# Performance work log

Measured on AMD Instinct MI355X. Metric: run time of the kernel, lower is better.

Reference implementation:

```python
import jax, jax.numpy as jnp
import numpy as np


def setup_inputs() -> dict:
    key = jax.random.key(0)
    x = jax.random.normal(key, (64, 2048, 512), dtype=jnp.float32)
    alpha = jnp.float32(0.2)
    beta = jnp.float32(0.1)
    return {"x": x, "alpha": alpha, "beta": beta}


def reference(x, alpha, beta):
    # x: [B, T, C]; double exponential smoothing recurrence over T.
    s0 = x[:, 0, :]                      # [B, C]
    b0 = x[:, 1, :] - s0                 # initial trend

    def step(carry, xt):
        s_prev, b = carry
        s = alpha * xt + (1.0 - alpha) * (s_prev + b)
        b = beta * (s - s_prev) + (1.0 - beta) * b
        return (s, b), s

    xs = jnp.swapaxes(x[:, 1:, :], 0, 1)           # [T-1, B, C]
    _, ss = jax.lax.scan(step, (s0, b0), xs)        # ss: [T-1, B, C]
    out = jnp.concatenate([s0[None], ss], axis=0)   # [T, B, C]
    return jnp.swapaxes(out, 0, 1)                  # [B, T, C]
```

## Files before the change

### kernel.cpp

```cpp
#include <hip/hip_runtime.h>


typedef float float4v __attribute__((ext_vector_type(4)));

constexpr int B      = 64;
constexpr int T      = 2048;
constexpr int F      = 512;
constexpr int NF4    = F / 4;
constexpr int CHUNKS = 8;
constexpr int W      = 64;
constexpr int LC     = (T - W) / CHUNKS;
constexpr int L0     = LC + W;

__device__ __forceinline__ float dema_step(float xv, float& s, float& bt,
                                           float alpha, float oma,
                                           float ab, float omab) {
  const float u  = fmaf(oma, bt, alpha * xv);
  const float sn = fmaf(oma, s, u);
  const float v  = fmaf(-ab, s, ab * xv);
  bt = fmaf(omab, bt, v);
  s  = sn;
  return sn;
}

__global__ __launch_bounds__(NF4) void dema_kernel(
    const float4v* __restrict__ x, float4v* __restrict__ out,
    const float* __restrict__ alpha_p, const float* __restrict__ beta_p) {
  const float alpha = alpha_p[0];
  const float beta  = beta_p[0];
  const float oma   = 1.0f - alpha;
  const float ab    = alpha * beta;
  const float omab  = 1.0f - ab;

  const int bidx = blockIdx.x;
  const int b    = bidx & (B - 1);
  const int c    = bidx >> 6;
  const int f4   = threadIdx.x;

  const float4v* __restrict__ xb = x   + (size_t)b * T * NF4 + f4;
  float4v* __restrict__       ob = out + (size_t)b * T * NF4 + f4;

  float s0, s1, s2, s3, b0, b1, b2, b3;
  int t, t_end;

  {
    const int tinit = (c == 0) ? 0 : (L0 + (c - 1) * LC - W);
    const float4v x0 = xb[(size_t)tinit * NF4];
    const float4v x1 = xb[(size_t)(tinit + 1) * NF4];
    s0 = x0.x; s1 = x0.y; s2 = x0.z; s3 = x0.w;
    b0 = x1.x - s0; b1 = x1.y - s1; b2 = x1.z - s2; b3 = x1.w - s3;
    if (c == 0) {
      __builtin_nontemporal_store(x0, &ob[0]);
      t_end = L0;
    } else {
      t_end = L0 + c * LC;
    }
    t = tinit + 1;
  }

  if (c > 0) {
    const int t_start = t_end - LC;
    #pragma unroll 8
    for (; t < t_start; ++t) {
      const float4v xv = xb[(size_t)t * NF4];
      dema_step(xv.x, s0, b0, alpha, oma, ab, omab);
      dema_step(xv.y, s1, b1, alpha, oma, ab, omab);
      dema_step(xv.z, s2, b2, alpha, oma, ab, omab);
      dema_step(xv.w, s3, b3, alpha, oma, ab, omab);
    }
  }

  #pragma unroll 8
  for (; t < t_end; ++t) {
    const float4v xv = xb[(size_t)t * NF4];
    float4v r;
    r.x = dema_step(xv.x, s0, b0, alpha, oma, ab, omab);
    r.y = dema_step(xv.y, s1, b1, alpha, oma, ab, omab);
    r.z = dema_step(xv.z, s2, b2, alpha, oma, ab, omab);
    r.w = dema_step(xv.w, s3, b3, alpha, oma, ab, omab);
    __builtin_nontemporal_store(r, &ob[(size_t)t * NF4]);
  }
}

extern "C" void kernel_launch(void* const* d_in, const int* in_sizes, int n_in,
                              void* d_out, int out_size, void* d_ws, size_t ws_size,
                              hipStream_t stream) {
  const float* x     = (const float*)d_in[0];
  const float* alpha = (const float*)d_in[1];
  const float* beta  = (const float*)d_in[2];
  float* out = (float*)d_out;

  dim3 grid(B * CHUNKS);
  dim3 block(NF4);
  dema_kernel<<<grid, block, 0, stream>>>(
      (const float4v*)x, (float4v*)out, alpha, beta);
}
```

Before: 474.0 us.

## Software-prefetch input rows and rebalance chunk geometry for uniform iteration count

Restructures the per-thread scan so that every chunk runs exactly the same number of iterations (warmup plus stored steps), merging the warmup and store loops into one loop with a predicated store. Adds an 8-deep register prefetch ring so loads for step t+8 are issued while step t computes, hiding global memory latency behind the serial recurrence. The warmup window grows from 64 to 111 steps, adding redundant recompute and extra reads in exchange for balanced work across blocks. The register buffer raises register use, and the clamped prefetch reads past the chunk end.

```diff
diff --git a/kernel.cpp b/kernel.cpp
--- a/kernel.cpp
+++ b/kernel.cpp
@@ -8,9 +8,14 @@
 constexpr int F      = 512;
 constexpr int NF4    = F / 4;
 constexpr int CHUNKS = 8;
-constexpr int W      = 64;
-constexpr int LC     = (T - W) / CHUNKS;
-constexpr int L0     = LC + W;
+constexpr int W      = 111;
+constexpr int NIT    = 352;
+constexpr int LC     = NIT - W + 1;
+constexpr int L0     = NIT + 2;
+static_assert(L0 + (CHUNKS - 1) * LC == T, "geometry");
+constexpr int PF     = 8;
+constexpr int NG     = NIT / PF;
+static_assert(NIT % PF == 0, "tail-free");
 
 __device__ __forceinline__ float dema_step(float xv, float& s, float& bt,
                                            float alpha, float oma,
@@ -41,44 +46,52 @@
   float4v* __restrict__       ob = out + (size_t)b * T * NF4 + f4;
 
   float s0, s1, s2, s3, b0, b1, b2, b3;
-  int t, t_end;
+  int t, t_store;
 
-  {
-    const int tinit = (c == 0) ? 0 : (L0 + (c - 1) * LC - W);
+  if (c == 0) {
+    const float4v x0 = xb[0];
+    const float4v x1 = xb[NF4];
+    s0 = x1.x; s1 = x1.y; s2 = x1.z; s3 = x1.w;
+    b0 = x1.x - x0.x; b1 = x1.y - x0.y; b2 = x1.z - x0.z; b3 = x1.w - x0.w;
+    __builtin_nontemporal_store(x0, &ob[0]);
+    __builtin_nontemporal_store(x1, &ob[NF4]);
+    t = 2;
+    t_store = 0;
+  } else {
+    const int cs    = L0 + (c - 1) * LC;
+    const int tinit = cs - W;
     const float4v x0 = xb[(size_t)tinit * NF4];
     const float4v x1 = xb[(size_t)(tinit + 1) * NF4];
     s0 = x0.x; s1 = x0.y; s2 = x0.z; s3 = x0.w;
     b0 = x1.x - s0; b1 = x1.y - s1; b2 = x1.z - s2; b3 = x1.w - s3;
-    if (c == 0) {
-      __builtin_nontemporal_store(x0, &ob[0]);
-      t_end = L0;
-    } else {
-      t_end = L0 + c * LC;
-    }
     t = tinit + 1;
+    t_store = cs;
   }
 
-  if (c > 0) {
-    const int t_start = t_end - LC;
-    #pragma unroll 8
-    for (; t < t_start; ++t) {
-      const float4v xv = xb[(size_t)t * NF4];
-      dema_step(xv.x, s0, b0, alpha, oma, ab, omab);
-      dema_step(xv.y, s1, b1, alpha, oma, ab, omab);
-      dema_step(xv.z, s2, b2, alpha, oma, ab, omab);
-      dema_step(xv.w, s3, b3, alpha, oma, ab, omab);
-    }
+  float4v buf[PF];
+  #pragma unroll
+  for (int j = 0; j < PF; ++j) {
+    int tl = t + j;
+    buf[j] = xb[(size_t)tl * NF4];
   }
 
-  #pragma unroll 8
-  for (; t < t_end; ++t) {
-    const float4v xv = xb[(size_t)t * NF4];
-    float4v r;
-    r.x = dema_step(xv.x, s0, b0, alpha, oma, ab, omab);
-    r.y = dema_step(xv.y, s1, b1, alpha, oma, ab, omab);
-    r.z = dema_step(xv.z, s2, b2, alpha, oma, ab, omab);
-    r.w = dema_step(xv.w, s3, b3, alpha, oma, ab, omab);
-    __builtin_nontemporal_store(r, &ob[(size_t)t * NF4]);
+  #pragma unroll 1
+  for (int g = 0; g < NG; ++g) {
+    #pragma unroll
+    for (int j = 0; j < PF; ++j) {
+      const float4v xv = buf[j];
+      float4v r;
+      r.x = dema_step(xv.x, s0, b0, alpha, oma, ab, omab);
+      r.y = dema_step(xv.y, s1, b1, alpha, oma, ab, omab);
+      r.z = dema_step(xv.z, s2, b2, alpha, oma, ab, omab);
+      r.w = dema_step(xv.w, s3, b3, alpha, oma, ab, omab);
+      if (t >= t_store)
+        __builtin_nontemporal_store(r, &ob[(size_t)t * NF4]);
+      int tl = t + PF;
+      if (tl > T - 1) tl = T - 1;
+      buf[j] = xb[(size_t)tl * NF4];
+      ++t;
+    }
   }
 }
 
```

Measured after the change: 469.8 us. No clear change (-0.9%).
